# Performance work log

Hardware: AMD Instinct MI355X
Metric: run time of the kernel (lower is better)

The kernel has to match this reference:

```python
import jax, jax.numpy as jnp
import numpy as np

N_HEADS = 16
ROPE_BASE = 10000.0


def apply_rope(x):
    # x: [B, H, T, D]; rotate interleaved pairs along last dim, positions along T
    B, H, T, D = x.shape
    half = D // 2
    inv_freq = 1.0 / (ROPE_BASE ** (jnp.arange(0, half, dtype=jnp.float32) * 2.0 / D))
    angles = jnp.arange(T, dtype=jnp.float32)[:, None] * inv_freq[None, :]  # [T, half]
    cos = jnp.cos(angles).astype(x.dtype)  # [T, half]
    sin = jnp.sin(angles).astype(x.dtype)
    xp = x.reshape(B, H, T, half, 2)
    x1, x2 = xp[..., 0], xp[..., 1]
    out = jnp.stack([x1 * cos - x2 * sin, x1 * sin + x2 * cos], axis=-1)
    return out.reshape(B, H, T, D)


def setup_inputs() -> dict:
    key = jax.random.key(0)
    k1, k2, k3 = jax.random.split(key, 3)
    C = 1024
    x = jax.random.normal(k1, (2, 2048, C), dtype=jnp.float32)
    w_qkv = jax.random.normal(k2, (C, 3 * C), dtype=jnp.float32) * (1.0 / np.sqrt(C))
    w_out = jax.random.normal(k3, (C, C), dtype=jnp.float32) * (1.0 / np.sqrt(C))
    return {"x": x, "w_qkv": w_qkv, "w_out": w_out}


def reference(x, w_qkv, w_out):
    B, T, C = x.shape
    H = N_HEADS
    D = C // H
    qkv = (x @ w_qkv).reshape(B, T, 3, H, D)
    q, k, v = qkv[:, :, 0], qkv[:, :, 1], qkv[:, :, 2]  # [B, T, H, D]
    q = jnp.transpose(q, (0, 2, 1, 3))  # [B, H, T, D]
    k = jnp.transpose(k, (0, 2, 1, 3))
    v = jnp.transpose(v, (0, 2, 1, 3))
    q = apply_rope(q)
    k = apply_rope(k)
    scale = 1.0 / np.sqrt(D)
    scores = jnp.einsum('bhqd,bhkd->bhqk', q, k) * scale
    causal = jnp.tril(jnp.ones((T, T), dtype=bool))
    scores = jnp.where(causal, scores, jnp.finfo(scores.dtype).min)
    attn = jax.nn.softmax(scores, axis=-1)
    out = jnp.einsum('bhqk,bhkd->bhqd', attn, v)  # [B, H, T, D]
    out = jnp.transpose(out, (0, 2, 1, 3)).reshape(B, T, C)
    return out @ w_out
```

## Files before the change

### kernel.cpp

```cpp
#include <hip/hip_runtime.h>
#include <hip/hip_bf16.h>

typedef __attribute__((ext_vector_type(8))) short v8s;
typedef __attribute__((ext_vector_type(4))) float v4f;
typedef __attribute__((ext_vector_type(16))) float v16f;

typedef const __attribute__((address_space(1))) void* gas_ptr;
typedef __attribute__((address_space(3))) void* las_ptr;

#define MFMA16(a, b, c) __builtin_amdgcn_mfma_f32_16x16x32_bf16((a), (b), (c), 0, 0, 0)
#define MFMA32(a, b, c) __builtin_amdgcn_mfma_f32_32x32x16_bf16((a), (b), (c), 0, 0, 0)

__device__ __forceinline__ void gload_lds16(const void* g, void* l) {
  __builtin_amdgcn_global_load_lds((gas_ptr)g, (las_ptr)l, 16, 0, 0);
}

__device__ __forceinline__ unsigned short f2bf(float f) {
  unsigned int u = __float_as_uint(f);
  u += 0x7FFFu + ((u >> 16) & 1u);
  return (unsigned short)(u >> 16);
}
__device__ __forceinline__ float bf2f(unsigned short h) {
  return __uint_as_float(((unsigned int)h) << 16);
}

__device__ __forceinline__ unsigned cvt_pk_bf16(float lo, float hi) {
  unsigned r;
  asm("v_cvt_pk_bf16_f32 %0, %1, %2" : "=v"(r) : "v"(lo), "v"(hi));
  return r;
}

__global__ __launch_bounds__(256) void k_convert(const float* __restrict__ in,
                                                 unsigned short* __restrict__ out, int n4) {
  int i = blockIdx.x * 256 + threadIdx.x;
  if (i >= n4) return;
  float4 v = ((const float4*)in)[i];
  ushort4 o;
  o.x = f2bf(v.x); o.y = f2bf(v.y); o.z = f2bf(v.z); o.w = f2bf(v.w);
  ((ushort4*)out)[i] = o;
}

__global__ __launch_bounds__(256) void k_transpose_convert(const float* __restrict__ in,
                                                           unsigned short* __restrict__ out,
                                                           int R, int C) {
  __shared__ __attribute__((aligned(16))) unsigned short tb[64 * 72];
  const int r0 = blockIdx.y * 64, c0 = blockIdx.x * 64;
  const int tid = threadIdx.x;
#pragma unroll
  for (int j = 0; j < 4; ++j) {
    int slot = tid + 256 * j;
    int row = slot >> 4, q4 = (slot & 15) * 4;
    float4 v = *(const float4*)&in[(size_t)(r0 + row) * C + c0 + q4];
    ushort4 o;
    o.x = f2bf(v.x); o.y = f2bf(v.y); o.z = f2bf(v.z); o.w = f2bf(v.w);
    *(ushort4*)&tb[row * 72 + q4] = o;
  }
  __syncthreads();
#pragma unroll
  for (int j = 0; j < 4; ++j) {
    int slot = tid + 256 * j;
    int crow = slot >> 4, t4 = (slot & 15) * 4;
    ushort4 o;
    o.x = tb[(t4 + 0) * 72 + crow];
    o.y = tb[(t4 + 1) * 72 + crow];
    o.z = tb[(t4 + 2) * 72 + crow];
    o.w = tb[(t4 + 3) * 72 + crow];
    *(ushort4*)&out[(size_t)(c0 + crow) * R + r0 + t4] = o;
  }
}

template <bool F32OUT, int BN, int WAVES_M, int WAVES_N>
__global__ __launch_bounds__(256) void k_gemm(const unsigned short* __restrict__ A,
                                              const unsigned short* __restrict__ Bt,
                                              void* __restrict__ Cout,
                                              int M, int N, int K) {
  constexpr int WM = 128 / (WAVES_M * 16);
  constexpr int WN = BN / (WAVES_N * 16);
  __shared__ __attribute__((aligned(16))) unsigned short As[128 * 32];
  __shared__ __attribute__((aligned(16))) unsigned short Bs[BN * 32];
  const int tid = threadIdx.x;
  const int w = tid >> 6, l = tid & 63, g = l >> 4, c = l & 15;
  const int wr = w / WAVES_N, wc = w % WAVES_N;

  const int nwg = gridDim.x * gridDim.y;
  const int orig = blockIdx.y * gridDim.x + blockIdx.x;
  const int wgid = (orig & 7) * (nwg >> 3) + (orig >> 3);
  const int mt = (wgid / gridDim.x) * 128;
  const int nt = (wgid % gridDim.x) * BN;

  const int rowc = l >> 2, kslot = (l & 3) * 8;

  v4f acc[WM][WN];
#pragma unroll
  for (int m = 0; m < WM; ++m)
#pragma unroll
    for (int n = 0; n < WN; ++n) acc[m][n] = (v4f){0.f, 0.f, 0.f, 0.f};

  constexpr int NCHUNK = 8 + BN / 16;
  for (int kt = 0; kt < K; kt += 32) {
    __syncthreads();
#pragma unroll
    for (int ch = 0; ch < NCHUNK; ch += 4) {
      int cc = ch + w;
      if (cc < 8)
        gload_lds16(&A[(size_t)(mt + cc * 16 + rowc) * K + kt + kslot], &As[cc * 512]);
      else
        gload_lds16(&Bt[(size_t)(nt + (cc - 8) * 16 + rowc) * K + kt + kslot],
                    &Bs[(cc - 8) * 512]);
    }
    __syncthreads();
    v8s af[WM], bfr[WN];
#pragma unroll
    for (int m = 0; m < WM; ++m)
      af[m] = *(const v8s*)&As[(wr * (WM * 16) + m * 16 + c) * 32 + g * 8];
#pragma unroll
    for (int n = 0; n < WN; ++n)
      bfr[n] = *(const v8s*)&Bs[(wc * (WN * 16) + n * 16 + c) * 32 + g * 8];
#pragma unroll
    for (int m = 0; m < WM; ++m)
#pragma unroll
      for (int n = 0; n < WN; ++n)
        acc[m][n] = MFMA16(af[m], bfr[n], acc[m][n]);
  }

#pragma unroll
  for (int m = 0; m < WM; ++m)
#pragma unroll
    for (int n = 0; n < WN; ++n)
#pragma unroll
      for (int r = 0; r < 4; ++r) {
        int row = mt + wr * (WM * 16) + m * 16 + g * 4 + r;
        int col = nt + wc * (WN * 16) + n * 16 + c;
        if (F32OUT)
          ((float*)Cout)[(size_t)row * N + col] = acc[m][n][r];
        else
          ((unsigned short*)Cout)[(size_t)row * N + col] = f2bf(acc[m][n][r]);
      }
}

__global__ __launch_bounds__(256) void k_post(const unsigned short* __restrict__ qkv,
                                              unsigned short* __restrict__ qp,
                                              unsigned short* __restrict__ kp,
                                              unsigned short* __restrict__ vp) {
  __shared__ float2 cs[64 * 32];
  __shared__ __attribute__((aligned(16))) unsigned short vt[64 * 72];
  const int bh = blockIdx.y;
  const int b = bh >> 4, hd = bh & 15;
  const int t0 = blockIdx.x * 64;
  const int tid = threadIdx.x;

#pragma unroll
  for (int e = 0; e < 8; ++e) {
    int idx = tid + 256 * e;
    int tl = idx >> 5, i = idx & 31;
    float invf = exp2f(-(float)i * 0.41524101186092034f);
    float ang = (float)(t0 + tl) * invf;
    float s, cc;
    sincosf(ang, &s, &cc);
    cs[idx] = make_float2(cc, s);
  }
#pragma unroll
  for (int j = 0; j < 2; ++j) {
    int slot = tid + 256 * j;
    int row = slot >> 3, c8 = (slot & 7) * 8;
    v8s vv = *(const v8s*)&qkv[(size_t)(b * 2048 + t0 + row) * 3072 + 2048 + hd * 64 + c8];
    *(v8s*)&vt[row * 72 + c8] = vv;
  }
  __syncthreads();

#pragma unroll
  for (int j = 0; j < 2; ++j) {
    int slot = tid + 256 * j;
    int row = slot >> 3, d0 = (slot & 7) * 8;
    int t = t0 + row;
    size_t base = (size_t)(b * 2048 + t) * 3072 + hd * 64;
    const int tile = t >> 5, c32 = t & 31, kd = d0 >> 4, hh = (d0 >> 3) & 1;
    const size_t pidx = (size_t)bh * 131072 + (tile * 4 + kd) * 512 + (hh * 32 + c32) * 8;
#pragma unroll
    for (int which = 0; which < 2; ++which) {
      const float qsc = which ? 1.0f : 0.18033688011112042f;
      v8s vq = *(const v8s*)&qkv[base + which * 1024 + d0];
      union { unsigned short s[8]; v8s v; } uo;
#pragma unroll
      for (int p = 0; p < 4; ++p) {
        float2 sc = cs[row * 32 + d0 / 2 + p];
        float x1 = bf2f((unsigned short)vq[2 * p]);
        float x2 = bf2f((unsigned short)vq[2 * p + 1]);
        uo.s[2 * p]     = f2bf((x1 * sc.x - x2 * sc.y) * qsc);
        uo.s[2 * p + 1] = f2bf((x1 * sc.y + x2 * sc.x) * qsc);
      }
      unsigned short* dst = which ? kp : qp;
      *(v8s*)&dst[pidx] = uo.v;
    }
  }

#pragma unroll
  for (int jj = 0; jj < 2; ++jj) {
    int idx = tid + 256 * jj;
    int tl = idx >> 8, kc = (idx >> 7) & 1, md = (idx >> 6) & 1;
    int lp = idx & 63, hh = lp >> 5, c32 = lp & 31;
    int d = md * 32 + c32;
    int brow = tl * 32 + kc * 16 + hh * 4;
    union { unsigned short s[8]; v8s v; } uo;
#pragma unroll
    for (int jh = 0; jh < 2; ++jh)
#pragma unroll
      for (int e = 0; e < 4; ++e)
        uo.s[jh * 4 + e] = vt[(brow + jh * 8 + e) * 72 + d];
    int tileG = (t0 >> 5) + tl;
    *(v8s*)&vp[(size_t)bh * 131072 + ((tileG * 2 + kc) * 2 + md) * 512 + lp * 8] = uo.v;
  }
}

__global__ __launch_bounds__(64) void k_attn(const unsigned short* __restrict__ qp,
                                             const unsigned short* __restrict__ kp,
                                             const unsigned short* __restrict__ vp,
                                             unsigned short* __restrict__ ao,
                                             char* __restrict__ part) {
  const int bid = (int)blockIdx.x;
  const int xcd = bid & 7, s2 = bid >> 3;
  const int bh = xcd + 8 * (s2 / 160);
  const int idx = 159 - (s2 % 160);
  int j, s;
  if (idx >= 96)      { j = 48 + ((idx - 96) >> 2); s = (idx - 96) & 3; }
  else if (idx >= 48) { j = 32 + (idx - 48) / 3;    s = (idx - 48) % 3; }
  else if (idx >= 16) { j = 16 + ((idx - 16) >> 1); s = (idx - 16) & 1; }
  else                { j = idx;                    s = 0; }
  const int t0 = s * 16;
  const int t1 = (t0 + 16 < j + 1) ? (t0 + 16) : (j + 1);

  const int l = threadIdx.x;
  const int c32 = l & 31, hh = l >> 5;
  const unsigned short* Qb = qp + (size_t)bh * 131072 + j * 4 * 512;
  const unsigned short* Kb = kp + (size_t)bh * 131072;
  const unsigned short* Vb = vp + (size_t)bh * 131072;

  v8s bq[4];
#pragma unroll
  for (int kd = 0; kd < 4; ++kd) bq[kd] = *(const v8s*)&Qb[kd * 512 + l * 8];

  v16f ot0 = {0,0,0,0,0,0,0,0,0,0,0,0,0,0,0,0};
  v16f ot1 = {0,0,0,0,0,0,0,0,0,0,0,0,0,0,0,0};
  float m2 = -1e30f, lsl = 0.f;

  v8s ak[2][4], av[2][2][2];
#pragma unroll
  for (int kd = 0; kd < 4; ++kd) ak[0][kd] = *(const v8s*)&Kb[((size_t)t0 * 4 + kd) * 512 + l * 8];
#pragma unroll
  for (int kc = 0; kc < 2; ++kc)
#pragma unroll
    for (int md = 0; md < 2; ++md)
      av[0][kc][md] = *(const v8s*)&Vb[(((size_t)t0 * 2 + kc) * 2 + md) * 512 + l * 8];
  if (t0 + 1 < t1) {
#pragma unroll
    for (int kd = 0; kd < 4; ++kd)
      ak[1][kd] = *(const v8s*)&Kb[((size_t)(t0 + 1) * 4 + kd) * 512 + l * 8];
#pragma unroll
    for (int kc = 0; kc < 2; ++kc)
#pragma unroll
      for (int md = 0; md < 2; ++md)
        av[1][kc][md] = *(const v8s*)&Vb[(((size_t)(t0 + 1) * 2 + kc) * 2 + md) * 512 + l * 8];
  }

  int t = t0;
  for (; t + 1 < t1; t += 2) {
    v16f st0 = {0,0,0,0,0,0,0,0,0,0,0,0,0,0,0,0};
    v16f st1 = {0,0,0,0,0,0,0,0,0,0,0,0,0,0,0,0};
    __builtin_amdgcn_s_setprio(1);
#pragma unroll
    for (int kd = 0; kd < 4; ++kd) {
      st0 = MFMA32(ak[0][kd], bq[kd], st0);
      st1 = MFMA32(ak[1][kd], bq[kd], st1);
    }
    __builtin_amdgcn_s_setprio(0);

    if (t + 2 < t1) {
#pragma unroll
      for (int kd = 0; kd < 4; ++kd)
        ak[0][kd] = *(const v8s*)&Kb[((size_t)(t + 2) * 4 + kd) * 512 + l * 8];
    }
    if (t + 3 < t1) {
#pragma unroll
      for (int kd = 0; kd < 4; ++kd)
        ak[1][kd] = *(const v8s*)&Kb[((size_t)(t + 3) * 4 + kd) * 512 + l * 8];
    }

    if (t + 1 == j) {
#pragma unroll
      for (int r = 0; r < 16; ++r) {
        int rloc = (r & 3) + 8 * (r >> 2) + 4 * hh;
        st1[r] = (rloc <= c32) ? st1[r] : -1e30f;
      }
    }

    float a0 = fmaxf(fmaxf(st0[0], st0[1]), fmaxf(st0[2], st0[3]));
    float a1 = fmaxf(fmaxf(st0[4], st0[5]), fmaxf(st0[6], st0[7]));
    float a2 = fmaxf(fmaxf(st0[8], st0[9]), fmaxf(st0[10], st0[11]));
    float a3 = fmaxf(fmaxf(st0[12], st0[13]), fmaxf(st0[14], st0[15]));
    float b0 = fmaxf(fmaxf(st1[0], st1[1]), fmaxf(st1[2], st1[3]));
    float b1 = fmaxf(fmaxf(st1[4], st1[5]), fmaxf(st1[6], st1[7]));
    float b2 = fmaxf(fmaxf(st1[8], st1[9]), fmaxf(st1[10], st1[11]));
    float b3 = fmaxf(fmaxf(st1[12], st1[13]), fmaxf(st1[14], st1[15]));
    float pm = fmaxf(fmaxf(fmaxf(a0, a1), fmaxf(a2, a3)),
                     fmaxf(fmaxf(b0, b1), fmaxf(b2, b3)));
    if (!__all(pm <= m2 + 8.f)) {
      float pmw = fmaxf(pm, __shfl_xor(pm, 32));
      float mn = fmaxf(m2, pmw);
      float al = exp2f(m2 - mn);
      m2 = mn;
      lsl *= al;
      ot0 *= al;
      ot1 *= al;
    }

#pragma unroll
    for (int r = 0; r < 16; ++r) st0[r] = exp2f(st0[r] - m2);
#pragma unroll
    for (int r = 0; r < 16; ++r) st1[r] = exp2f(st1[r] - m2);
    {
      float e0 = (st0[0] + st0[1]) + (st0[2] + st0[3]);
      float e1 = (st0[4] + st0[5]) + (st0[6] + st0[7]);
      float e2 = (st0[8] + st0[9]) + (st0[10] + st0[11]);
      float e3 = (st0[12] + st0[13]) + (st0[14] + st0[15]);
      float f0 = (st1[0] + st1[1]) + (st1[2] + st1[3]);
      float f1 = (st1[4] + st1[5]) + (st1[6] + st1[7]);
      float f2 = (st1[8] + st1[9]) + (st1[10] + st1[11]);
      float f3 = (st1[12] + st1[13]) + (st1[14] + st1[15]);
      lsl += ((e0 + e1) + (e2 + e3)) + ((f0 + f1) + (f2 + f3));
    }

    unsigned wd0[8], wd1[8];
#pragma unroll
    for (int i = 0; i < 8; ++i) wd0[i] = cvt_pk_bf16(st0[2 * i], st0[2 * i + 1]);
#pragma unroll
    for (int i = 0; i < 8; ++i) wd1[i] = cvt_pk_bf16(st1[2 * i], st1[2 * i + 1]);
    union { unsigned u[4]; v8s v; } p00, p01, p10, p11;
    p00.u[0] = wd0[0]; p00.u[1] = wd0[1]; p00.u[2] = wd0[2]; p00.u[3] = wd0[3];
    p01.u[0] = wd0[4]; p01.u[1] = wd0[5]; p01.u[2] = wd0[6]; p01.u[3] = wd0[7];
    p10.u[0] = wd1[0]; p10.u[1] = wd1[1]; p10.u[2] = wd1[2]; p10.u[3] = wd1[3];
    p11.u[0] = wd1[4]; p11.u[1] = wd1[5]; p11.u[2] = wd1[6]; p11.u[3] = wd1[7];

    __builtin_amdgcn_s_setprio(1);
    ot0 = MFMA32(av[0][0][0], p00.v, ot0);
    ot1 = MFMA32(av[0][0][1], p00.v, ot1);
    ot0 = MFMA32(av[0][1][0], p01.v, ot0);
    ot1 = MFMA32(av[0][1][1], p01.v, ot1);
    ot0 = MFMA32(av[1][0][0], p10.v, ot0);
    ot1 = MFMA32(av[1][0][1], p10.v, ot1);
    ot0 = MFMA32(av[1][1][0], p11.v, ot0);
    ot1 = MFMA32(av[1][1][1], p11.v, ot1);
    __builtin_amdgcn_s_setprio(0);

    if (t + 2 < t1) {
#pragma unroll
      for (int kc = 0; kc < 2; ++kc)
#pragma unroll
        for (int md = 0; md < 2; ++md)
          av[0][kc][md] = *(const v8s*)&Vb[(((size_t)(t + 2) * 2 + kc) * 2 + md) * 512 + l * 8];
    }
    if (t + 3 < t1) {
#pragma unroll
      for (int kc = 0; kc < 2; ++kc)
#pragma unroll
        for (int md = 0; md < 2; ++md)
          av[1][kc][md] = *(const v8s*)&Vb[(((size_t)(t + 3) * 2 + kc) * 2 + md) * 512 + l * 8];
    }
  }

  if (t < t1) {
    v16f st = {0,0,0,0,0,0,0,0,0,0,0,0,0,0,0,0};
    __builtin_amdgcn_s_setprio(1);
#pragma unroll
    for (int kd = 0; kd < 4; ++kd) st = MFMA32(ak[0][kd], bq[kd], st);
    __builtin_amdgcn_s_setprio(0);

    if (t == j) {
#pragma unroll
      for (int r = 0; r < 16; ++r) {
        int rloc = (r & 3) + 8 * (r >> 2) + 4 * hh;
        st[r] = (rloc <= c32) ? st[r] : -1e30f;
      }
    }

    float a0 = fmaxf(fmaxf(st[0], st[1]), fmaxf(st[2], st[3]));
    float a1 = fmaxf(fmaxf(st[4], st[5]), fmaxf(st[6], st[7]));
    float a2 = fmaxf(fmaxf(st[8], st[9]), fmaxf(st[10], st[11]));
    float a3 = fmaxf(fmaxf(st[12], st[13]), fmaxf(st[14], st[15]));
    float pm = fmaxf(fmaxf(a0, a1), fmaxf(a2, a3));
    if (!__all(pm <= m2 + 8.f)) {
      float pmw = fmaxf(pm, __shfl_xor(pm, 32));
      float mn = fmaxf(m2, pmw);
      float al = exp2f(m2 - mn);
      m2 = mn;
      lsl *= al;
      ot0 *= al;
      ot1 *= al;
    }
#pragma unroll
    for (int r = 0; r < 16; ++r) st[r] = exp2f(st[r] - m2);
    float e0 = (st[0] + st[1]) + (st[2] + st[3]);
    float e1 = (st[4] + st[5]) + (st[6] + st[7]);
    float e2 = (st[8] + st[9]) + (st[10] + st[11]);
    float e3 = (st[12] + st[13]) + (st[14] + st[15]);
    lsl += (e0 + e1) + (e2 + e3);

    unsigned wd[8];
#pragma unroll
    for (int i = 0; i < 8; ++i) wd[i] = cvt_pk_bf16(st[2 * i], st[2 * i + 1]);
    union { unsigned u[4]; v8s v; } pb0, pb1;
    pb0.u[0] = wd[0]; pb0.u[1] = wd[1]; pb0.u[2] = wd[2]; pb0.u[3] = wd[3];
    pb1.u[0] = wd[4]; pb1.u[1] = wd[5]; pb1.u[2] = wd[6]; pb1.u[3] = wd[7];

    __builtin_amdgcn_s_setprio(1);
    ot0 = MFMA32(av[0][0][0], pb0.v, ot0);
    ot1 = MFMA32(av[0][0][1], pb0.v, ot1);
    ot0 = MFMA32(av[0][1][0], pb1.v, ot0);
    ot1 = MFMA32(av[0][1][1], pb1.v, ot1);
    __builtin_amdgcn_s_setprio(0);
  }

  const float ls = lsl + __shfl_xor(lsl, 32);
  const float inv = 1.f / ls;
  if (j < 16) {
    const int b = bh >> 4, hd = bh & 15;
    const int tq = j * 32 + c32;
    unsigned short* aop = ao + (size_t)(b * 2048 + tq) * 1024 + hd * 64;
#pragma unroll
    for (int md = 0; md < 2; ++md)
#pragma unroll
      for (int q = 0; q < 4; ++q) {
        const v16f& o = md ? ot1 : ot0;
        unsigned w0 = cvt_pk_bf16(o[4 * q + 0] * inv, o[4 * q + 1] * inv);
        unsigned w1 = cvt_pk_bf16(o[4 * q + 2] * inv, o[4 * q + 3] * inv);
        int d = md * 32 + 8 * q + 4 * hh;
        *(uint2*)&aop[d] = make_uint2(w0, w1);
      }
  } else {
    char* slot = part + ((size_t)bh * 160 + idx) * 4352;
#pragma unroll
    for (int md = 0; md < 2; ++md)
#pragma unroll
      for (int i = 0; i < 8; ++i) {
        const v16f& o = md ? ot1 : ot0;
        union { _Float16 h[2]; unsigned u; } pk;
        pk.h[0] = (_Float16)(o[2 * i] * inv);
        pk.h[1] = (_Float16)(o[2 * i + 1] * inv);
        *(unsigned*)(slot + ((md * 8 + i) * 64 + l) * 4) = pk.u;
      }
    if (hh == 0) {
      *(float*)(slot + 4096 + c32 * 4) = m2;
      *(float*)(slot + 4224 + c32 * 4) = ls;
    }
  }
}

__global__ __launch_bounds__(64) void k_comb(const char* __restrict__ part,
                                             unsigned short* __restrict__ ao) {
  const int bh = blockIdx.y;
  const int j = 16 + (int)blockIdx.x;
  const int g = j >> 4;
  const int nch = g + 1;
  const int l = threadIdx.x, c32 = l & 31, hh = l >> 5;
  const int baseg = (g == 1) ? 16 : (g == 2) ? 48 : 96;
  const int ord0 = baseg + (j - 16 * g) * nch;
  const char* base = part + (size_t)bh * 160 * 4352;

  float ms[4], lsv[4], wsc[4];
  float mfin = -1e30f;
#pragma unroll
  for (int s = 0; s < 4; ++s) {
    if (s < nch) {
      const char* sl = base + (size_t)(ord0 + s) * 4352;
      ms[s] = *(const float*)(sl + 4096 + c32 * 4);
      lsv[s] = *(const float*)(sl + 4224 + c32 * 4);
      mfin = fmaxf(mfin, ms[s]);
    }
  }
  float lfin = 0.f;
#pragma unroll
  for (int s = 0; s < 4; ++s) {
    if (s < nch) {
      wsc[s] = lsv[s] * exp2f(ms[s] - mfin);
      lfin += wsc[s];
    }
  }
  const float inv = 1.f / lfin;
#pragma unroll
  for (int s = 0; s < 4; ++s)
    if (s < nch) wsc[s] *= inv;

  const int b = bh >> 4, hd = bh & 15;
  const int t = j * 32 + c32;
  unsigned short* aop = ao + (size_t)(b * 2048 + t) * 1024 + hd * 64;
#pragma unroll
  for (int md = 0; md < 2; ++md)
#pragma unroll
    for (int q4 = 0; q4 < 4; ++q4) {
      const int w0 = md * 8 + 2 * q4;
      float a0 = 0.f, a1 = 0.f, a2 = 0.f, a3 = 0.f;
#pragma unroll
      for (int s = 0; s < 4; ++s) {
        if (s < nch) {
          const char* sl = base + (size_t)(ord0 + s) * 4352;
          unsigned u0 = *(const unsigned*)(sl + ((w0 + 0) * 64 + l) * 4);
          unsigned u1 = *(const unsigned*)(sl + ((w0 + 1) * 64 + l) * 4);
          union { unsigned u; _Float16 h[2]; } p0, p1;
          p0.u = u0; p1.u = u1;
          a0 += (float)p0.h[0] * wsc[s];
          a1 += (float)p0.h[1] * wsc[s];
          a2 += (float)p1.h[0] * wsc[s];
          a3 += (float)p1.h[1] * wsc[s];
        }
      }
      unsigned o0 = cvt_pk_bf16(a0, a1);
      unsigned o1 = cvt_pk_bf16(a2, a3);
      int d = md * 32 + 8 * q4 + 4 * hh;
      *(uint2*)&aop[d] = make_uint2(o0, o1);
    }
}

extern "C" void kernel_launch(void* const* d_in, const int* in_sizes, int n_in,
                              void* d_out, int out_size, void* d_ws, size_t ws_size,
                              hipStream_t stream) {
  const float* x     = (const float*)d_in[0];
  const float* w_qkv = (const float*)d_in[1];
  const float* w_out = (const float*)d_in[2];
  float* out = (float*)d_out;

  char* ws = (char*)d_ws;
  unsigned short* xbf = (unsigned short*)(ws);
  unsigned short* wqT = (unsigned short*)(ws + 8388608);
  unsigned short* woT = (unsigned short*)(ws + 14680064);
  unsigned short* qkv = (unsigned short*)(ws + 16777216);
  unsigned short* qp  = (unsigned short*)(ws + 41943040);
  unsigned short* kp  = (unsigned short*)(ws + 50331648);
  unsigned short* vp  = (unsigned short*)(ws + 58720256);
  char* part = (char*)(ws + 16777216);

  k_convert<<<4096, 256, 0, stream>>>(x, xbf, 1048576);
  k_transpose_convert<<<dim3(48, 16), 256, 0, stream>>>(w_qkv, wqT, 1024, 3072);
  k_transpose_convert<<<dim3(16, 16), 256, 0, stream>>>(w_out, woT, 1024, 1024);
  k_gemm<false, 128, 2, 2><<<dim3(24, 32), 256, 0, stream>>>(xbf, wqT, qkv, 4096, 3072, 1024);
  k_post<<<dim3(32, 32), 256, 0, stream>>>(qkv, qp, kp, vp);
  k_attn<<<5120, 64, 0, stream>>>(qp, kp, vp, xbf , part);
  k_comb<<<dim3(48, 32), 64, 0, stream>>>(part, xbf);
  k_gemm<true, 64, 4, 1><<<dim3(16, 32), 256, 0, stream>>>(xbf, woT, (void*)out, 4096, 1024, 1024);
}
```

Measured before the change: 139.6 us.

## Fuse RoPE and QKV repacking into QKV GEMM epilogue via shared-memory tile

The QKV projection GEMM now stages its 128x128 output tile in LDS and directly applies RoPE and q-scaling, writing q/k/v in the attention-friendly packed layouts. This removes the separate k_post kernel and the round trip of the full qkv intermediate through global memory. The sin/cos table is precomputed once by extra blocks appended to the convert kernel and read from global memory. The larger LDS footprint (about 50KB) may reduce GEMM occupancy, and the specialized GEMM uses a simple non-pipelined K loop.

```diff
diff --git a/kernel.cpp b/kernel.cpp
--- a/kernel.cpp
+++ b/kernel.cpp
@@ -31,7 +31,22 @@
 }
 
 __global__ __launch_bounds__(256) void k_convert(const float* __restrict__ in,
-                                                 unsigned short* __restrict__ out, int n4) {
+                                                 unsigned short* __restrict__ out,
+                                                 float2* __restrict__ tab, int n4) {
+  if ((int)blockIdx.x >= 4096) {
+    int base = ((int)blockIdx.x - 4096) * 256 + threadIdx.x;
+#pragma unroll
+    for (int e = 0; e < 8; ++e) {
+      int n = base * 8 + e;
+      int pos = n >> 5, i = n & 31;
+      float invf = exp2f(-(float)i * 0.41524101186092034f);
+      float ang = (float)pos * invf;
+      float s, cc;
+      sincosf(ang, &s, &cc);
+      tab[n] = make_float2(cc, s);
+    }
+    return;
+  }
   int i = blockIdx.x * 256 + threadIdx.x;
   if (i >= n4) return;
   float4 v = ((const float4*)in)[i];
@@ -138,77 +153,119 @@
       }
 }
 
-__global__ __launch_bounds__(256) void k_post(const unsigned short* __restrict__ qkv,
-                                              unsigned short* __restrict__ qp,
-                                              unsigned short* __restrict__ kp,
-                                              unsigned short* __restrict__ vp) {
-  __shared__ float2 cs[64 * 32];
-  __shared__ __attribute__((aligned(16))) unsigned short vt[64 * 72];
-  const int bh = blockIdx.y;
-  const int b = bh >> 4, hd = bh & 15;
-  const int t0 = blockIdx.x * 64;
+__global__ __launch_bounds__(256) void k_gemm_qkv(const unsigned short* __restrict__ A,
+                                                  const unsigned short* __restrict__ Bt,
+                                                  const float2* __restrict__ tab,
+                                                  unsigned short* __restrict__ qp,
+                                                  unsigned short* __restrict__ kp,
+                                                  unsigned short* __restrict__ vp) {
+  __shared__ __attribute__((aligned(16))) unsigned short As[128 * 32];
+  __shared__ __attribute__((aligned(16))) unsigned short Bs[128 * 32];
+  __shared__ __attribute__((aligned(16))) unsigned short T[128 * 136];
   const int tid = threadIdx.x;
-
-#pragma unroll
-  for (int e = 0; e < 8; ++e) {
-    int idx = tid + 256 * e;
-    int tl = idx >> 5, i = idx & 31;
-    float invf = exp2f(-(float)i * 0.41524101186092034f);
-    float ang = (float)(t0 + tl) * invf;
-    float s, cc;
-    sincosf(ang, &s, &cc);
-    cs[idx] = make_float2(cc, s);
-  }
-#pragma unroll
-  for (int j = 0; j < 2; ++j) {
-    int slot = tid + 256 * j;
-    int row = slot >> 3, c8 = (slot & 7) * 8;
-    v8s vv = *(const v8s*)&qkv[(size_t)(b * 2048 + t0 + row) * 3072 + 2048 + hd * 64 + c8];
-    *(v8s*)&vt[row * 72 + c8] = vv;
-  }
+  const int w = tid >> 6, l = tid & 63, g = l >> 4, c = l & 15;
+  const int wr = w >> 1, wc = w & 1;
+
+  const int nwg = 768;
+  const int orig = blockIdx.y * 24 + blockIdx.x;
+  const int wgid = (orig & 7) * (nwg >> 3) + (orig >> 3);
+  const int mt = (wgid / 24) * 128;
+  const int nt = (wgid % 24) * 128;
+
+  const int rowc = l >> 2, kslot = (l & 3) * 8;
+
+  v4f acc[4][4];
+#pragma unroll
+  for (int m = 0; m < 4; ++m)
+#pragma unroll
+    for (int n = 0; n < 4; ++n) acc[m][n] = (v4f){0.f, 0.f, 0.f, 0.f};
+
+  for (int kt = 0; kt < 1024; kt += 32) {
+    __syncthreads();
+#pragma unroll
+    for (int ch = 0; ch < 16; ch += 4) {
+      int cc = ch + w;
+      if (cc < 8)
+        gload_lds16(&A[(size_t)(mt + cc * 16 + rowc) * 1024 + kt + kslot], &As[cc * 512]);
+      else
+        gload_lds16(&Bt[(size_t)(nt + (cc - 8) * 16 + rowc) * 1024 + kt + kslot],
+                    &Bs[(cc - 8) * 512]);
+    }
+    __syncthreads();
+    v8s af[4], bfr[4];
+#pragma unroll
+    for (int m = 0; m < 4; ++m)
+      af[m] = *(const v8s*)&As[(wr * 64 + m * 16 + c) * 32 + g * 8];
+#pragma unroll
+    for (int n = 0; n < 4; ++n)
+      bfr[n] = *(const v8s*)&Bs[(wc * 64 + n * 16 + c) * 32 + g * 8];
+#pragma unroll
+    for (int m = 0; m < 4; ++m)
+#pragma unroll
+      for (int n = 0; n < 4; ++n)
+        acc[m][n] = MFMA16(af[m], bfr[n], acc[m][n]);
+  }
+
+#pragma unroll
+  for (int m = 0; m < 4; ++m)
+#pragma unroll
+    for (int n = 0; n < 4; ++n)
+#pragma unroll
+      for (int r = 0; r < 4; ++r)
+        T[(wr * 64 + m * 16 + g * 4 + r) * 136 + wc * 64 + n * 16 + c] = f2bf(acc[m][n][r]);
   __syncthreads();
 
-#pragma unroll
-  for (int j = 0; j < 2; ++j) {
-    int slot = tid + 256 * j;
-    int row = slot >> 3, d0 = (slot & 7) * 8;
-    int t = t0 + row;
-    size_t base = (size_t)(b * 2048 + t) * 3072 + hd * 64;
-    const int tile = t >> 5, c32 = t & 31, kd = d0 >> 4, hh = (d0 >> 3) & 1;
-    const size_t pidx = (size_t)bh * 131072 + (tile * 4 + kd) * 512 + (hh * 32 + c32) * 8;
-#pragma unroll
-    for (int which = 0; which < 2; ++which) {
-      const float qsc = which ? 1.0f : 0.18033688011112042f;
-      v8s vq = *(const v8s*)&qkv[base + which * 1024 + d0];
+  const int which = nt >> 10;
+  const int h0 = (nt & 1023) >> 6;
+  const int b = mt >> 11;
+  const int posbase = mt & 2047;
+
+  if (which < 2) {
+    const float qsc = which ? 1.0f : 0.18033688011112042f;
+    unsigned short* dst = which ? kp : qp;
+#pragma unroll
+    for (int it = 0; it < 8; ++it) {
+      int task = it * 256 + tid;
+      int c32t = task & 31;
+      int grp = task >> 5;
+      int hg = grp & 1, kd = (grp >> 1) & 3, tR = (grp >> 3) & 3, hd2 = grp >> 5;
+      int row = tR * 32 + c32t;
+      int d0 = kd * 16 + hg * 8;
+      int pos = posbase + row;
+      v8s vq = *(const v8s*)&T[row * 136 + hd2 * 64 + d0];
       union { unsigned short s[8]; v8s v; } uo;
 #pragma unroll
       for (int p = 0; p < 4; ++p) {
-        float2 sc = cs[row * 32 + d0 / 2 + p];
+        float2 sc = tab[pos * 32 + (d0 >> 1) + p];
         float x1 = bf2f((unsigned short)vq[2 * p]);
         float x2 = bf2f((unsigned short)vq[2 * p + 1]);
         uo.s[2 * p]     = f2bf((x1 * sc.x - x2 * sc.y) * qsc);
         uo.s[2 * p + 1] = f2bf((x1 * sc.y + x2 * sc.x) * qsc);
       }
-      unsigned short* dst = which ? kp : qp;
-      *(v8s*)&dst[pidx] = uo.v;
-    }
-  }
-
-#pragma unroll
-  for (int jj = 0; jj < 2; ++jj) {
-    int idx = tid + 256 * jj;
-    int tl = idx >> 8, kc = (idx >> 7) & 1, md = (idx >> 6) & 1;
-    int lp = idx & 63, hh = lp >> 5, c32 = lp & 31;
-    int d = md * 32 + c32;
-    int brow = tl * 32 + kc * 16 + hh * 4;
-    union { unsigned short s[8]; v8s v; } uo;
-#pragma unroll
-    for (int jh = 0; jh < 2; ++jh)
-#pragma unroll
-      for (int e = 0; e < 4; ++e)
-        uo.s[jh * 4 + e] = vt[(brow + jh * 8 + e) * 72 + d];
-    int tileG = (t0 >> 5) + tl;
-    *(v8s*)&vp[(size_t)bh * 131072 + ((tileG * 2 + kc) * 2 + md) * 512 + lp * 8] = uo.v;
+      int bh = b * 16 + h0 + hd2;
+      int tileG = pos >> 5;
+      *(v8s*)&dst[(size_t)bh * 131072 + (tileG * 4 + kd) * 512 + (hg * 32 + c32t) * 8] = uo.v;
+    }
+  } else {
+#pragma unroll
+    for (int it = 0; it < 8; ++it) {
+      int task = it * 256 + tid;
+      int lp = task & 63;
+      int grp = task >> 6;
+      int md = grp & 1, kc = (grp >> 1) & 1, tR = (grp >> 2) & 3, hd2 = grp >> 4;
+      int hh2 = lp >> 5, c32d = lp & 31;
+      int d = md * 32 + c32d;
+      int brow = tR * 32 + kc * 16 + hh2 * 4;
+      union { unsigned short s[8]; v8s v; } uo;
+#pragma unroll
+      for (int jh = 0; jh < 2; ++jh)
+#pragma unroll
+        for (int e = 0; e < 4; ++e)
+          uo.s[jh * 4 + e] = T[(brow + jh * 8 + e) * 136 + hd2 * 64 + d];
+      int bh = b * 16 + h0 + hd2;
+      int tileG = (posbase >> 5) + tR;
+      *(v8s*)&vp[(size_t)bh * 131072 + ((tileG * 2 + kc) * 2 + md) * 512 + lp * 8] = uo.v;
+    }
   }
 }
 
@@ -531,17 +588,16 @@
   unsigned short* xbf = (unsigned short*)(ws);
   unsigned short* wqT = (unsigned short*)(ws + 8388608);
   unsigned short* woT = (unsigned short*)(ws + 14680064);
-  unsigned short* qkv = (unsigned short*)(ws + 16777216);
+  float2* tab = (float2*)(ws + 16777216);
+  char* part = (char*)(ws + 16777216);
   unsigned short* qp  = (unsigned short*)(ws + 41943040);
   unsigned short* kp  = (unsigned short*)(ws + 50331648);
   unsigned short* vp  = (unsigned short*)(ws + 58720256);
-  char* part = (char*)(ws + 16777216);
-
-  k_convert<<<4096, 256, 0, stream>>>(x, xbf, 1048576);
+
+  k_convert<<<4128, 256, 0, stream>>>(x, xbf, tab, 1048576);
   k_transpose_convert<<<dim3(48, 16), 256, 0, stream>>>(w_qkv, wqT, 1024, 3072);
   k_transpose_convert<<<dim3(16, 16), 256, 0, stream>>>(w_out, woT, 1024, 1024);
-  k_gemm<false, 128, 2, 2><<<dim3(24, 32), 256, 0, stream>>>(xbf, wqT, qkv, 4096, 3072, 1024);
-  k_post<<<dim3(32, 32), 256, 0, stream>>>(qkv, qp, kp, vp);
+  k_gemm_qkv<<<dim3(24, 32), 256, 0, stream>>>(xbf, wqT, tab, qp, kp, vp);
   k_attn<<<5120, 64, 0, stream>>>(qp, kp, vp, xbf , part);
   k_comb<<<dim3(48, 32), 64, 0, stream>>>(part, xbf);
   k_gemm<true, 64, 4, 1><<<dim3(16, 32), 256, 0, stream>>>(xbf, woT, (void*)out, 4096, 1024, 1024);
```

Result: faster. 133.3 us (-4.5%).
